# Optimization experiments

Hardware: AMD Instinct MI355X
Metric: run time of the kernel (lower is better)

Reference implementation:

```python
import jax, jax.numpy as jnp
import numpy as np

B, T, H, YD, L, IN = 128, 1024, 256, 30, 3, 6


def setup_inputs() -> dict:
    key = jax.random.key(0)
    ks = jax.random.split(key, 32)
    s = 1.0 / np.sqrt(H)

    def u(k, shape):
        return jax.random.uniform(k, shape, jnp.float32, -s, s)

    inp = {
        "rew": jax.random.normal(ks[0], (B, T), jnp.float32),
        "done": (jax.random.uniform(ks[1], (B, T)) < 0.02).astype(jnp.float32),
        "gamma": jnp.array([0.99], jnp.float32),
        "prob": jax.random.uniform(ks[2], (B, T), jnp.float32),
        "y": jax.random.uniform(ks[3], (B, T, YD), jnp.float32),
        "y1": jax.random.uniform(ks[4], (B, T, YD), jnp.float32),
    }
    dims = [IN, H, H]
    for l in range(L):
        inp[f"w_ih{l}"] = u(ks[5 + 4 * l], (3 * H, dims[l]))
        inp[f"w_hh{l}"] = u(ks[6 + 4 * l], (3 * H, H))
        inp[f"b_ih{l}"] = u(ks[7 + 4 * l], (3 * H,))
        inp[f"b_hh{l}"] = u(ks[8 + 4 * l], (3 * H,))
    inp["w_fc_y"] = u(ks[20], (YD, H)); inp["b_fc_y"] = u(ks[21], (YD,))
    inp["w_fc_pi"] = u(ks[22], (1, H)); inp["b_fc_pi"] = u(ks[23], (1,))
    inp["w_e1"] = u(ks[24], (16, YD)); inp["b_e1"] = u(ks[25], (16,))
    inp["w_e2"] = u(ks[26], (1, 16)); inp["b_e2"] = u(ks[27], (1,))
    return inp


def _forward(rew, done, gamma, prob, y, y1,
             w_ih0, w_hh0, b_ih0, b_hh0,
             w_ih1, w_hh1, b_ih1, b_hh1,
             w_ih2, w_hh2, b_ih2, b_hh2,
             w_fc_y, b_fc_y, w_fc_pi, b_fc_pi,
             w_e1, b_e1, w_e2, b_e2):
    def embed(v):  # embed_y: Linear -> relu -> Linear -> sigmoid, [B,T,YD]->[B,T,1]
        h1 = jax.nn.relu(v @ w_e1.T + b_e1)
        return jax.nn.sigmoid(h1 @ w_e2.T + b_e2)

    fi_y = embed(y)
    fi_y1 = embed(y1)
    g = gamma * jnp.ones((B, T, 1), rew.dtype)
    x = jnp.concatenate([rew[..., None], done[..., None], g,
                         prob[..., None], fi_y, fi_y1], axis=-1)  # [B,T,6]
    x = jnp.flip(x, axis=1)  # reverse time, as in torch.flip(input, dims=[1])
    xs = jnp.moveaxis(x, 1, 0)  # [T,B,6]
    ds = xs[:, :, 1:2]          # done channel, [T,B,1]

    wih = (w_ih0, w_ih1, w_ih2)
    whh = (w_hh0, w_hh1, w_hh2)
    bih = (b_ih0, b_ih1, b_ih2)
    bhh = (b_hh0, b_hh1, b_hh2)

    def cell(xt, h, Wi, Wh, bi, bh):  # PyTorch GRU cell math
        gi = xt @ Wi.T + bi
        gh = h @ Wh.T + bh
        ir, iz, inn = jnp.split(gi, 3, axis=-1)
        hr, hz, hn = jnp.split(gh, 3, axis=-1)
        r = jax.nn.sigmoid(ir + hr)
        z = jax.nn.sigmoid(iz + hz)
        n = jnp.tanh(inn + r * hn)
        return (1.0 - z) * n + z * h

    def step(h, xd):
        xt, dt = xd                       # xt [B,6], dt [B,1]
        h = h * (1.0 - dt)[None]          # reset hidden where done==1
        layer_in = xt
        hs = []
        for l in range(L):
            hl = cell(layer_in, h[l], wih[l], whh[l], bih[l], bhh[l])
            hs.append(hl)
            layer_in = hl
        return jnp.stack(hs), layer_in

    h0 = jnp.zeros((L, B, H), xs.dtype)
    _, out = jax.lax.scan(step, h0, (xs, ds))  # out [T,B,H]
    out = jnp.moveaxis(out, 0, 1)              # [B,T,H]

    yo = jax.nn.sigmoid(out @ w_fc_y.T + b_fc_y)  # [B,T,YD]
    pi = out @ w_fc_pi.T + b_fc_pi                # [B,T,1]
    pi = jnp.flip(pi, axis=1)[..., 0]             # [B,T]
    yo = jnp.flip(yo, axis=1)                     # [B,T,YD] (squeeze(-1) is a no-op for YD>1)
    return pi, yo


def reference(rew, done, gamma, prob, y, y1,
              w_ih0, w_hh0, b_ih0, b_hh0,
              w_ih1, w_hh1, b_ih1, b_hh1,
              w_ih2, w_hh2, b_ih2, b_hh2,
              w_fc_y, b_fc_y, w_fc_pi, b_fc_pi,
              w_e1, b_e1, w_e2, b_e2):
    return _forward(rew, done, gamma, prob, y, y1,
                    w_ih0, w_hh0, b_ih0, b_hh0,
                    w_ih1, w_hh1, b_ih1, b_hh1,
                    w_ih2, w_hh2, b_ih2, b_hh2,
                    w_fc_y, b_fc_y, w_fc_pi, b_fc_pi,
                    w_e1, b_e1, w_e2, b_e2)
```

## Files before the change

### kernel.cpp

```cpp
#include <hip/hip_runtime.h>

#define BDIM 128
#define TDIM 1024
#define HDIM 256
#define SLOT (BDIM*HDIM)
#define NWG_TOTAL 208
#define RING 14

#define FLAGS_OFF 0u
#define HD_OFF    8192u
#define XF_OFF    5513216u
#define DONEF_OFF 8658944u
#define WS_NEEDED 9183232u
#define NZERO_U32 1378304

#define LDSW_BYTES 61440
#define LDS_DYN    122880

typedef __attribute__((ext_vector_type(8))) short bf16x8;
typedef __attribute__((ext_vector_type(4))) float f32x4;

static __device__ __forceinline__ unsigned short f2bf(float f) {
  union { float f; unsigned u; } v; v.f = f;
  unsigned r = v.u + 0x7fffu + ((v.u >> 16) & 1u);
  return (unsigned short)(r >> 16);
}
static __device__ __forceinline__ float bf2f(unsigned short h) {
  union { unsigned u; float f; } v; v.u = ((unsigned)h) << 16;
  return v.f;
}
static __device__ __forceinline__ float sigm(float x) { return 1.f / (1.f + __expf(-x)); }
static __device__ __forceinline__ float tanha(float x) { return 1.f - 2.f / (1.f + __expf(2.f * x)); }

static __device__ __forceinline__ unsigned long long ld_u64_coh(const void* p) {
  return __hip_atomic_load((const unsigned long long*)p, __ATOMIC_RELAXED, __HIP_MEMORY_SCOPE_AGENT);
}
static __device__ __forceinline__ void st_u32_coh(void* p, unsigned v) {
  __hip_atomic_store((unsigned*)p, v, __ATOMIC_RELAXED, __HIP_MEMORY_SCOPE_AGENT);
}

static __device__ __forceinline__ bf16x8 ld16_coh_nowait(const unsigned short* p) {
  bf16x8 v;
  asm volatile("global_load_dwordx4 %0, %1, off sc0 sc1" : "=v"(v) : "v"(p));
  return v;
}
template <int N>
static __device__ __forceinline__ void wait_vm() {
  asm volatile("s_waitcnt vmcnt(%0)" :: "i"(N) : "memory");
  __builtin_amdgcn_sched_barrier(0);
}

static __device__ __forceinline__ unsigned poll_flag(const unsigned* p) {
  return __hip_atomic_load(p, __ATOMIC_RELAXED, __HIP_MEMORY_SCOPE_AGENT);
}
static __device__ __forceinline__ void post_flag(unsigned* fl, int g, int w, int s1) {
  (void)__hip_atomic_exchange(fl + (g * 16 + w) * 8, (unsigned)s1,
                              __ATOMIC_RELAXED, __HIP_MEMORY_SCOPE_AGENT);
}

static __device__ __forceinline__ void wave_wait2(unsigned* fl,
                                                  int g0, int t0, int skip0,
                                                  int g1, int t1,
                                                  int g2, int t2, bool g2four) {
  const int lane = threadIdx.x & 63;
  const int sel = lane >> 4;
  const int w = lane & 15;
  int g = g0, tgt = t0;
  if (sel == 1) { g = g1; tgt = t1; }
  if (sel == 2) { g = g2; tgt = t2; }
  if (sel == 3) tgt = 0;
  if (sel == 0 && w == skip0) tgt = 0;
  const int wi = (sel == 2 && g2four) ? (w & 3) : w;
  const unsigned* p = fl + (g * 16 + wi) * 8;
  const bool need = tgt > 0;
  for (;;) {
    int ok = 1;
    if (need) ok = ((int)poll_flag(p) >= tgt);
    if (__all(ok)) break;
    __builtin_amdgcn_s_sleep(8);
  }
  asm volatile("" ::: "memory");
}

__global__ void diag_kernel(float* out, float code) {
  if (threadIdx.x == 0 && blockIdx.x == 0) out[0] = code;
}

__global__ void prep_kernel(const float* __restrict__ rew, const float* __restrict__ done,
                            const float* __restrict__ gamma, const float* __restrict__ prob,
                            const float* __restrict__ y, const float* __restrict__ y1,
                            const float* __restrict__ w_e1, const float* __restrict__ b_e1,
                            const float* __restrict__ w_e2, const float* __restrict__ b_e2,
                            char* __restrict__ ws) {
  unsigned* zbase = (unsigned*)ws;
  float* donef = (float*)(ws + DONEF_OFF);
  float* xfeat = (float*)(ws + XF_OFF);

  __shared__ float we1[480], be1[16], we2[16];
  __shared__ float be2s, gam;
  for (int i = threadIdx.x; i < 480; i += blockDim.x) we1[i] = w_e1[i];
  if (threadIdx.x < 16) { be1[threadIdx.x] = b_e1[threadIdx.x]; we2[threadIdx.x] = w_e2[threadIdx.x]; }
  if (threadIdx.x == 0) { be2s = b_e2[0]; gam = gamma[0]; }
  __syncthreads();
  const int gid = blockIdx.x * blockDim.x + threadIdx.x;
  const int stride = gridDim.x * blockDim.x;

  for (int i = gid; i < NZERO_U32; i += stride) zbase[i] = 0u;
  for (int i = gid; i < BDIM * TDIM; i += stride) donef[i] = done[i];

  for (int i = gid; i < BDIM * TDIM; i += stride) {
    float yr[30], y1r[30];
    #pragma unroll
    for (int c = 0; c < 30; ++c) { yr[c] = y[(size_t)i * 30 + c]; y1r[c] = y1[(size_t)i * 30 + c]; }
    float a0 = 0.f, a1 = 0.f;
    #pragma unroll 4
    for (int jm = 0; jm < 16; ++jm) {
      float s0 = be1[jm], s1 = be1[jm];
      #pragma unroll
      for (int c = 0; c < 30; ++c) { float w = we1[jm * 30 + c]; s0 += yr[c] * w; s1 += y1r[c] * w; }
      a0 += fmaxf(s0, 0.f) * we2[jm];
      a1 += fmaxf(s1, 0.f) * we2[jm];
    }
    float* xr = xfeat + (size_t)i * 6;
    xr[0] = rew[i]; xr[1] = done[i]; xr[2] = gam;
    xr[3] = prob[i]; xr[4] = sigm(a0 + be2s); xr[5] = sigm(a1 + be2s);
  }
}

template <bool L0T>
__device__ __forceinline__ void layer_body(int l, int rg, int js, char* __restrict__ ws,
                                           char* __restrict__ ldsW,
                                           char* __restrict__ ldsX,
                                           const float* __restrict__ Wh,
                                           const float* __restrict__ Wx,
                                           const float* __restrict__ bi,
                                           const float* __restrict__ bh,
                                           const float* __restrict__ wi0) {
  unsigned short* hd = (unsigned short*)(ws + HD_OFF);
  unsigned* fl = (unsigned*)(ws + FLAGS_OFF);
  const float* donef = (const float*)(ws + DONEF_OFF);
  const float* xfeat = (const float*)(ws + XF_OFF);

  const int tid = threadIdx.x;
  const int wv = tid >> 6, lane = tid & 63, q = lane >> 4, jj = lane & 15;
  const int j = js * 16 + jj;

  const float bi_r = bi[j], bi_z = bi[256 + j], bi_n = bi[512 + j];
  const float bh_r = bh[j], bh_z = bh[256 + j], bh_n = bh[512 + j];

  for (int idx = tid; idx < 12288; idx += 128) {
    const int row = idx >> 8, k = idx & 255;
    const int g = row >> 4, jr = row & 15;
    const float w = Wh[(size_t)(g * 256 + js * 16 + jr) * 256 + k];
    const unsigned short d1 = f2bf(w);
    const unsigned short d2 = f2bf(w - bf2f(d1));
    const int itc = k >> 5, kk = k & 31;
    *(unsigned short*)(ldsW + ((g * 2 + 0) * 8 + itc) * 1280 + jr * 80 + kk * 2) = d1;
    *(unsigned short*)(ldsW + ((g * 2 + 1) * 8 + itc) * 1280 + jr * 80 + kk * 2) = d2;
  }
  if (!L0T) {
    for (int idx = tid; idx < 12288; idx += 128) {
      const int row = idx >> 8, k = idx & 255;
      const int g = row >> 4, jr = row & 15;
      const float w = Wx[(size_t)(g * 256 + js * 16 + jr) * 256 + k];
      const unsigned short d1 = f2bf(w);
      const unsigned short d2 = f2bf(w - bf2f(d1));
      const int itc = k >> 5, kk = k & 31;
      *(unsigned short*)(ldsX + ((g * 2 + 0) * 8 + itc) * 1280 + jr * 80 + kk * 2) = d1;
      *(unsigned short*)(ldsX + ((g * 2 + 1) * 8 + itc) * 1280 + jr * 80 + kk * 2) = d2;
    }
  }
  __syncthreads();

  float wx0[3][6];
  if (L0T) {
    #pragma unroll
    for (int g = 0; g < 3; ++g)
      #pragma unroll
      for (int c = 0; c < 6; ++c) wx0[g][c] = wi0[(g * 256 + j) * 6 + c];
  }

  float hc[4];
  #pragma unroll
  for (int i = 0; i < 4; ++i) hc[i] = 0.f;

  const int mA = (rg * 2 + wv) * 16 + jj;
  const f32x4 z4 = {0.f, 0.f, 0.f, 0.f};

  for (int s = 0; s < 1024; ++s) {
    const int t = 1023 - s;
    const int pc = s % RING, pp = (s + RING - 1) % RING;

    float sFv[4];
    #pragma unroll
    for (int i = 0; i < 4; ++i)
      sFv[i] = 1.f - donef[((rg * 2 + wv) * 16 + q * 4 + i) * TDIM + t];

    if (L0T)         wave_wait2(fl, rg,     s, js, 4 + rg,  s - (RING - 1), 0, 0, false);
    else if (l == 1) wave_wait2(fl, 4 + rg, s, js, rg,      s + 1, 8 + rg,  s - (RING - 1), false);
    else             wave_wait2(fl, 8 + rg, s, js, 4 + rg,  s + 1, 12 + rg, s - (RING - 1), true);

    const unsigned short* hh1 = hd + (size_t)((l * RING + pp) * 2 + 0) * SLOT;
    const unsigned short* hh2 = hd + (size_t)((l * RING + pp) * 2 + 1) * SLOT;
    const unsigned short* hx1 = L0T ? (const unsigned short*)0 : hd + (size_t)(((l - 1) * RING + pc) * 2 + 0) * SLOT;
    const unsigned short* hx2 = L0T ? (const unsigned short*)0 : hd + (size_t)(((l - 1) * RING + pc) * 2 + 1) * SLOT;
    unsigned short* hdw1 = hd + (size_t)((l * RING + pc) * 2 + 0) * SLOT;
    unsigned short* hdw2 = hd + (size_t)((l * RING + pc) * 2 + 1) * SLOT;

    bf16x8 A1[8], A2[8], X1[8], X2[8];
    #pragma unroll
    for (int it = 0; it < 8; ++it) {
      const size_t ro = (size_t)mA * 256 + it * 32 + q * 8;
      A1[it] = ld16_coh_nowait(hh1 + ro);
      A2[it] = ld16_coh_nowait(hh2 + ro);
    }
    if (!L0T) {
      #pragma unroll
      for (int it = 0; it < 8; ++it) {
        const size_t ro = (size_t)mA * 256 + it * 32 + q * 8;
        X1[it] = ld16_coh_nowait(hx1 + ro);
        X2[it] = ld16_coh_nowait(hx2 + ro);
      }
    }

    f32x4 Ch[3], Cx[3];
    #pragma unroll
    for (int g = 0; g < 3; ++g) { Ch[g] = z4; Cx[g] = z4; }

    if (L0T) wait_vm<0>(); else wait_vm<16>();
    #pragma unroll
    for (int it = 0; it < 8; ++it) {
      const int cb = it * 1280 + jj * 80 + q * 16;
      #pragma unroll
      for (int g = 0; g < 3; ++g) {
        #pragma unroll
        for (int dig = 0; dig < 2; ++dig) {
          const bf16x8 wb = *(const bf16x8*)(ldsW + ((g * 2 + dig) * 8) * 1280 + cb);
          Ch[g] = __builtin_amdgcn_mfma_f32_16x16x32_bf16(A1[it], wb, Ch[g], 0, 0, 0);
          Ch[g] = __builtin_amdgcn_mfma_f32_16x16x32_bf16(A2[it], wb, Ch[g], 0, 0, 0);
        }
      }
    }
    if (!L0T) {
      wait_vm<0>();
      #pragma unroll
      for (int it = 0; it < 8; ++it) {
        const int cb = it * 1280 + jj * 80 + q * 16;
        #pragma unroll
        for (int g = 0; g < 3; ++g) {
          #pragma unroll
          for (int dig = 0; dig < 2; ++dig) {
            const bf16x8 xb = *(const bf16x8*)(ldsX + ((g * 2 + dig) * 8) * 1280 + cb);
            Cx[g] = __builtin_amdgcn_mfma_f32_16x16x32_bf16(X1[it], xb, Cx[g], 0, 0, 0);
            Cx[g] = __builtin_amdgcn_mfma_f32_16x16x32_bf16(X2[it], xb, Cx[g], 0, 0, 0);
          }
        }
      }
    }

    #pragma unroll
    for (int i = 0; i < 4; ++i) {
      const int mC = (rg * 2 + wv) * 16 + q * 4 + i;
      const float sF = sFv[i];
      float gxr, gxz, gxn;
      if (L0T) {
        const float* xr = xfeat + ((size_t)mC * TDIM + t) * 6;
        gxr = 0.f; gxz = 0.f; gxn = 0.f;
        #pragma unroll
        for (int c = 0; c < 6; ++c) {
          const float xv = xr[c];
          gxr += xv * wx0[0][c]; gxz += xv * wx0[1][c]; gxn += xv * wx0[2][c];
        }
      } else {
        gxr = Cx[0][i]; gxz = Cx[1][i]; gxn = Cx[2][i];
      }
      const float r = sigm(gxr + bi_r + sF * Ch[0][i] + bh_r);
      const float z = sigm(gxz + bi_z + sF * Ch[1][i] + bh_z);
      const float n = tanha(gxn + bi_n + r * (sF * Ch[2][i] + bh_n));
      const float hp = hc[i] * sF;
      const float hv = (1.f - z) * n + z * hp;
      hc[i] = hv;
      const unsigned short d1 = f2bf(hv);
      const unsigned short d2 = f2bf(hv - bf2f(d1));
      const int o1 = __shfl_xor((int)d1, 1, 64);
      const int o2 = __shfl_xor((int)d2, 1, 64);
      const unsigned val = (jj & 1) ? ((unsigned)(o2 & 0xffff) | ((unsigned)d2 << 16))
                                    : ((unsigned)d1 | ((unsigned)(o1 & 0xffff) << 16));
      unsigned short* bp = ((jj & 1) ? hdw2 : hdw1) + (size_t)mC * 256 + (j & ~1);
      st_u32_coh(bp, val);
    }

    asm volatile("s_waitcnt vmcnt(0)" ::: "memory");
    __syncthreads();
    if (tid == 0) post_flag(fl, l * 4 + rg, js, s + 1);
  }
}

__device__ __forceinline__ void head_body(int hw, char* __restrict__ ws, float* __restrict__ out,
                                          char* __restrict__ lds,
                                          const float* __restrict__ wfy,
                                          const float* __restrict__ bfy,
                                          const float* __restrict__ wfp,
                                          const float* __restrict__ bfp) {
  const unsigned short* hd = (const unsigned short*)(ws + HD_OFF);
  unsigned* fl = (unsigned*)(ws + FLAGS_OFF);
  float* hlds = (float*)lds;

  const int tid = threadIdx.x;
  const int rg = hw >> 2;

  for (int s = 0; s < 1024; ++s) {
    const int t = 1023 - s;
    const int pc = s % RING;
    wave_wait2(fl, 8 + rg, s + 1, -1, 0, 0, 0, 0, false);

    #pragma unroll
    for (int sub = 0; sub < 2; ++sub) {
      const int te = tid + 128 * sub;
      const size_t rowoff = (size_t)(hw * 8 + (te >> 5)) * 256 + (te & 31) * 8;
      const unsigned short* p1 = hd + (size_t)((2 * RING + pc) * 2 + 0) * SLOT + rowoff;
      const unsigned short* p2 = hd + (size_t)((2 * RING + pc) * 2 + 1) * SLOT + rowoff;
      unsigned long long q10 = ld_u64_coh(p1);
      unsigned long long q11 = ld_u64_coh(p1 + 4);
      unsigned long long q20 = ld_u64_coh(p2);
      unsigned long long q21 = ld_u64_coh(p2 + 4);
      float* dst = hlds + (te >> 5) * 256 + (te & 31) * 8;
      #pragma unroll
      for (int e = 0; e < 4; ++e) {
        dst[e]     = bf2f((unsigned short)(q10 >> (16 * e))) + bf2f((unsigned short)(q20 >> (16 * e)));
        dst[4 + e] = bf2f((unsigned short)(q11 >> (16 * e))) + bf2f((unsigned short)(q21 >> (16 * e)));
      }
    }
    __syncthreads();
    #pragma unroll
    for (int sub = 0; sub < 2; ++sub) {
      const int te = tid + 128 * sub;
      const int d = te & 31;
      const int bb = te >> 5;
      const int b = hw * 8 + bb;
      if (d < 31) {
        const float* wrow = (d < 30) ? (wfy + d * 256) : wfp;
        const float biasv = (d < 30) ? bfy[d] : bfp[0];
        const float* hr = hlds + bb * 256;
        float a0 = 0.f, a1 = 0.f;
        #pragma unroll 8
        for (int kk = 0; kk < 256; kk += 8) {
          const f32x4 h0 = *(const f32x4*)(hr + kk);
          const f32x4 h1 = *(const f32x4*)(hr + kk + 4);
          const f32x4 w0 = *(const f32x4*)(wrow + kk);
          const f32x4 w1 = *(const f32x4*)(wrow + kk + 4);
          a0 += h0[0]*w0[0] + h0[1]*w0[1] + h0[2]*w0[2] + h0[3]*w0[3];
          a1 += h1[0]*w1[0] + h1[1]*w1[1] + h1[2]*w1[2] + h1[3]*w1[3];
        }
        const float acc = a0 + a1;
        if (d < 30) out[BDIM * TDIM + ((size_t)b * TDIM + t) * 30 + d] = sigm(acc + biasv);
        else        out[(size_t)b * TDIM + t] = acc + biasv;
      }
    }
    __syncthreads();
    if (tid == 0) post_flag(fl, 12 + rg, hw & 3, s + 1);
  }
}

__global__ void __launch_bounds__(128, 1) gru_main(char* __restrict__ ws,
                                                   float* __restrict__ out,
                                                   const float* __restrict__ wi0,
                                                   const float* __restrict__ wh0,
                                                   const float* __restrict__ bi0,
                                                   const float* __restrict__ bh0,
                                                   const float* __restrict__ wi1,
                                                   const float* __restrict__ wh1,
                                                   const float* __restrict__ bi1,
                                                   const float* __restrict__ bh1,
                                                   const float* __restrict__ wi2,
                                                   const float* __restrict__ wh2,
                                                   const float* __restrict__ bi2,
                                                   const float* __restrict__ bh2,
                                                   const float* __restrict__ wfy,
                                                   const float* __restrict__ bfy,
                                                   const float* __restrict__ wfp,
                                                   const float* __restrict__ bfp) {
  extern __shared__ char lds[];
  const int bid = blockIdx.x;
  if (bid < 192) {
    const int l = bid >> 6;
    const int rg = (bid >> 4) & 3;
    const int js = bid & 15;
    const float* Wh = (l == 0) ? wh0 : (l == 1) ? wh1 : wh2;
    const float* Wx = (l == 0) ? (const float*)0 : (l == 1) ? wi1 : wi2;
    const float* bi = (l == 0) ? bi0 : (l == 1) ? bi1 : bi2;
    const float* bh = (l == 0) ? bh0 : (l == 1) ? bh1 : bh2;
    if (l == 0) layer_body<true>(l, rg, js, ws, lds, lds + LDSW_BYTES, Wh, Wx, bi, bh, wi0);
    else        layer_body<false>(l, rg, js, ws, lds, lds + LDSW_BYTES, Wh, Wx, bi, bh, wi0);
  } else {
    head_body(bid - 192, ws, out, lds, wfy, bfy, wfp, bfp);
  }
}

extern "C" void kernel_launch(void* const* d_in, const int* in_sizes, int n_in,
                              void* d_out, int out_size, void* d_ws, size_t ws_size,
                              hipStream_t stream) {
  static const int EXP_SIZES[26] = {131072, 131072, 1, 131072, 3932160, 3932160,
                                    4608, 196608, 768, 768,
                                    196608, 196608, 768, 768,
                                    196608, 196608, 768, 768,
                                    7680, 30, 256, 1, 480, 16, 16, 1};
  float code = 0.f;
  if (n_in != 26) code = 900.f;
  if (code == 0.f) {
    for (int i = 0; i < 26; ++i)
      if (in_sizes[i] != EXP_SIZES[i]) { code = 100.f + 4.f * (float)i; break; }
  }
  if (code == 0.f && out_size != 4063232) code = 400.f;
  if (code == 0.f && ws_size < (size_t)WS_NEEDED) code = 300.f;
  if (code != 0.f) {
    diag_kernel<<<1, 64, 0, stream>>>((float*)d_out, code);
    return;
  }

  static int attr_done = 0;
  if (!attr_done) {
    attr_done = 1;
    (void)hipFuncSetAttribute((const void*)gru_main,
                              hipFuncAttributeMaxDynamicSharedMemorySize, LDS_DYN);
  }

  char* ws = (char*)d_ws;
  prep_kernel<<<512, 256, 0, stream>>>(
      (const float*)d_in[0], (const float*)d_in[1], (const float*)d_in[2],
      (const float*)d_in[3], (const float*)d_in[4], (const float*)d_in[5],
      (const float*)d_in[22], (const float*)d_in[23], (const float*)d_in[24], (const float*)d_in[25],
      ws);
  gru_main<<<NWG_TOTAL, 128, LDS_DYN, stream>>>(
      ws, (float*)d_out,
      (const float*)d_in[6], (const float*)d_in[7], (const float*)d_in[8], (const float*)d_in[9],
      (const float*)d_in[10], (const float*)d_in[11], (const float*)d_in[12], (const float*)d_in[13],
      (const float*)d_in[14], (const float*)d_in[15], (const float*)d_in[16], (const float*)d_in[17],
      (const float*)d_in[18], (const float*)d_in[19], (const float*)d_in[20], (const float*)d_in[21]);
}
```

Before: 9.002 ms.

## Start per-chunk hidden-state loads as soon as producer flags become ready

The old code waited for every producer workgroup flag before issuing any hidden-state loads. It is replaced by a per-wave ballot of own-layer and upstream flags. Each K-chunk of the recurrent and input GEMM is loaded as soon as the two producer workgroups covering that chunk have posted, and up to two chunks are prefetched ahead with matching vmcnt waits. This lets MFMA work on ready chunks overlap with waiting on slower producers, which shortens the critical path per timestep. The cost is more polling traffic, more complex control flow with possible divergence, and a risk of subtle ordering bugs in the vmcnt accounting.

```diff
diff --git a/kernel.cpp b/kernel.cpp
--- a/kernel.cpp
+++ b/kernel.cpp
@@ -56,6 +56,34 @@
 static __device__ __forceinline__ void post_flag(unsigned* fl, int g, int w, int s1) {
   (void)__hip_atomic_exchange(fl + (g * 16 + w) * 8, (unsigned)s1,
                               __ATOMIC_RELAXED, __HIP_MEMORY_SCOPE_AGENT);
+}
+
+static __device__ __forceinline__ void bp_wait(unsigned* fl, int g, int tgt, bool four) {
+  if (tgt <= 0) return;
+  const int lane = threadIdx.x & 63;
+  for (;;) {
+    int ok = 1;
+    if (lane < 16) {
+      const int wi = four ? (lane & 3) : lane;
+      ok = ((int)poll_flag(fl + (g * 16 + wi) * 8) >= tgt);
+    }
+    if (__all(ok)) break;
+    __builtin_amdgcn_s_sleep(8);
+  }
+  asm volatile("" ::: "memory");
+}
+
+static __device__ __forceinline__ unsigned long long poll_round(
+    unsigned* fl, int gOwn, int sOwn, int js, int gUp, int sUp, bool l0t) {
+  const int lane = threadIdx.x & 63;
+  int ok = 1;
+  if (lane < 16) {
+    if (lane != js && sOwn > 0)
+      ok = ((int)poll_flag(fl + (gOwn * 16 + lane) * 8) >= sOwn);
+  } else if (lane < 32 && !l0t) {
+    ok = ((int)poll_flag(fl + (gUp * 16 + (lane - 16)) * 8) >= sUp);
+  }
+  return __ballot(ok);
 }
 
 static __device__ __forceinline__ void wave_wait2(unsigned* fl,
@@ -186,6 +214,10 @@
 
   const int mA = (rg * 2 + wv) * 16 + jj;
   const f32x4 z4 = {0.f, 0.f, 0.f, 0.f};
+  const int gOwn = l * 4 + rg;
+  const int gUp  = L0T ? 0 : (l - 1) * 4 + rg;
+  const int gDn  = (l == 2) ? (12 + rg) : (l + 1) * 4 + rg;
+  const bool dn4 = (l == 2);
 
   for (int s = 0; s < 1024; ++s) {
     const int t = 1023 - s;
@@ -196,9 +228,8 @@
     for (int i = 0; i < 4; ++i)
       sFv[i] = 1.f - donef[((rg * 2 + wv) * 16 + q * 4 + i) * TDIM + t];
 
-    if (L0T)         wave_wait2(fl, rg,     s, js, 4 + rg,  s - (RING - 1), 0, 0, false);
-    else if (l == 1) wave_wait2(fl, 4 + rg, s, js, rg,      s + 1, 8 + rg,  s - (RING - 1), false);
-    else             wave_wait2(fl, 8 + rg, s, js, 4 + rg,  s + 1, 12 + rg, s - (RING - 1), true);
+    bp_wait(fl, gDn, s - (RING - 1), dn4);
+    unsigned long long M = poll_round(fl, gOwn, s, js, gUp, s + 1, L0T);
 
     const unsigned short* hh1 = hd + (size_t)((l * RING + pp) * 2 + 0) * SLOT;
     const unsigned short* hh2 = hd + (size_t)((l * RING + pp) * 2 + 1) * SLOT;
@@ -207,54 +238,79 @@
     unsigned short* hdw1 = hd + (size_t)((l * RING + pc) * 2 + 0) * SLOT;
     unsigned short* hdw2 = hd + (size_t)((l * RING + pc) * 2 + 1) * SLOT;
 
+    f32x4 Ch[3], Cx[3];
+    #pragma unroll
+    for (int g = 0; g < 3; ++g) { Ch[g] = z4; Cx[g] = z4; }
+
     bf16x8 A1[8], A2[8], X1[8], X2[8];
+    unsigned ism = 0;
+
+    auto canp = [&](int p) -> bool {
+      const unsigned own = (unsigned)((M >> (2 * p)) & 3ull);
+      const unsigned up  = (unsigned)((M >> (16 + 2 * p)) & 3ull);
+      return own == 3u && up == 3u;
+    };
+
     #pragma unroll
     for (int it = 0; it < 8; ++it) {
-      const size_t ro = (size_t)mA * 256 + it * 32 + q * 8;
-      A1[it] = ld16_coh_nowait(hh1 + ro);
-      A2[it] = ld16_coh_nowait(hh2 + ro);
-    }
-    if (!L0T) {
-      #pragma unroll
-      for (int it = 0; it < 8; ++it) {
-        const size_t ro = (size_t)mA * 256 + it * 32 + q * 8;
-        X1[it] = ld16_coh_nowait(hx1 + ro);
-        X2[it] = ld16_coh_nowait(hx2 + ro);
-      }
-    }
-
-    f32x4 Ch[3], Cx[3];
-    #pragma unroll
-    for (int g = 0; g < 3; ++g) { Ch[g] = z4; Cx[g] = z4; }
-
-    if (L0T) wait_vm<0>(); else wait_vm<16>();
-    #pragma unroll
-    for (int it = 0; it < 8; ++it) {
-      const int cb = it * 1280 + jj * 80 + q * 16;
-      #pragma unroll
-      for (int g = 0; g < 3; ++g) {
-        #pragma unroll
-        for (int dig = 0; dig < 2; ++dig) {
-          const bf16x8 wb = *(const bf16x8*)(ldsW + ((g * 2 + dig) * 8) * 1280 + cb);
-          Ch[g] = __builtin_amdgcn_mfma_f32_16x16x32_bf16(A1[it], wb, Ch[g], 0, 0, 0);
-          Ch[g] = __builtin_amdgcn_mfma_f32_16x16x32_bf16(A2[it], wb, Ch[g], 0, 0, 0);
-        }
-      }
-    }
-    if (!L0T) {
-      wait_vm<0>();
-      #pragma unroll
-      for (int it = 0; it < 8; ++it) {
+      if (!((ism >> it) & 1u)) {
+        while (!canp(it)) {
+          __builtin_amdgcn_s_sleep(1);
+          M = poll_round(fl, gOwn, s, js, gUp, s + 1, L0T);
+        }
+        {
+          const size_t ro = (size_t)mA * 256 + it * 32 + q * 8;
+          A1[it] = ld16_coh_nowait(hh1 + ro);
+          A2[it] = ld16_coh_nowait(hh2 + ro);
+          if constexpr (!L0T) { X1[it] = ld16_coh_nowait(hx1 + ro); X2[it] = ld16_coh_nowait(hx2 + ro); }
+        }
+        ism |= 1u << it;
+      }
+      {
+        const int y = ((it + 1 < 8) ? (int)((ism >> (it + 1)) & 1u) : 0)
+                    + ((it + 2 < 8) ? (int)((ism >> (it + 2)) & 1u) : 0);
+        if (y == 0) wait_vm<0>();
+        else if (y == 1) { if constexpr (L0T) wait_vm<2>(); else wait_vm<4>(); }
+        else             { if constexpr (L0T) wait_vm<4>(); else wait_vm<8>(); }
+      }
+      {
         const int cb = it * 1280 + jj * 80 + q * 16;
         #pragma unroll
         for (int g = 0; g < 3; ++g) {
           #pragma unroll
           for (int dig = 0; dig < 2; ++dig) {
-            const bf16x8 xb = *(const bf16x8*)(ldsX + ((g * 2 + dig) * 8) * 1280 + cb);
-            Cx[g] = __builtin_amdgcn_mfma_f32_16x16x32_bf16(X1[it], xb, Cx[g], 0, 0, 0);
-            Cx[g] = __builtin_amdgcn_mfma_f32_16x16x32_bf16(X2[it], xb, Cx[g], 0, 0, 0);
+            const bf16x8 wb = *(const bf16x8*)(ldsW + ((g * 2 + dig) * 8) * 1280 + cb);
+            Ch[g] = __builtin_amdgcn_mfma_f32_16x16x32_bf16(A1[it], wb, Ch[g], 0, 0, 0);
+            Ch[g] = __builtin_amdgcn_mfma_f32_16x16x32_bf16(A2[it], wb, Ch[g], 0, 0, 0);
           }
         }
+        if constexpr (!L0T) {
+          #pragma unroll
+          for (int g = 0; g < 3; ++g) {
+            #pragma unroll
+            for (int dig = 0; dig < 2; ++dig) {
+              const bf16x8 xb = *(const bf16x8*)(ldsX + ((g * 2 + dig) * 8) * 1280 + cb);
+              Cx[g] = __builtin_amdgcn_mfma_f32_16x16x32_bf16(X1[it], xb, Cx[g], 0, 0, 0);
+              Cx[g] = __builtin_amdgcn_mfma_f32_16x16x32_bf16(X2[it], xb, Cx[g], 0, 0, 0);
+            }
+          }
+        }
+      }
+      if (it + 1 < 8 && !((ism >> (it + 1)) & 1u) && canp(it + 1)) {
+        const int c1 = it + 1;
+        const size_t ro = (size_t)mA * 256 + c1 * 32 + q * 8;
+        A1[c1] = ld16_coh_nowait(hh1 + ro);
+        A2[c1] = ld16_coh_nowait(hh2 + ro);
+        if constexpr (!L0T) { X1[c1] = ld16_coh_nowait(hx1 + ro); X2[c1] = ld16_coh_nowait(hx2 + ro); }
+        ism |= 1u << c1;
+      }
+      if (it + 2 < 8 && ((ism >> (it + 1)) & 1u) && !((ism >> (it + 2)) & 1u) && canp(it + 2)) {
+        const int c2 = it + 2;
+        const size_t ro = (size_t)mA * 256 + c2 * 32 + q * 8;
+        A1[c2] = ld16_coh_nowait(hh1 + ro);
+        A2[c2] = ld16_coh_nowait(hh2 + ro);
+        if constexpr (!L0T) { X1[c2] = ld16_coh_nowait(hx1 + ro); X2[c2] = ld16_coh_nowait(hx2 + ro); }
+        ism |= 1u << c2;
       }
     }
 
@@ -292,7 +348,7 @@
 
     asm volatile("s_waitcnt vmcnt(0)" ::: "memory");
     __syncthreads();
-    if (tid == 0) post_flag(fl, l * 4 + rg, js, s + 1);
+    if (tid == 0) post_flag(fl, gOwn, js, s + 1);
   }
 }
 
```

New measurement: 8.915 ms. Within noise of the previous version (-1.0%).
